# Performance work log

Hardware: AMD Instinct MI355X
Metric: run time of the kernel (lower is better)

The kernel has to match this reference:

```python
import jax, jax.numpy as jnp
import numpy as np

RES = 96
CENTER = RES // 2
EPS = 1e-5


def setup_inputs() -> dict:
    key = jax.random.key(0)
    boundary_2d = jax.random.normal(key, (RES, RES), dtype=jnp.float32)
    return {"boundary_2d": boundary_2d}


def reference(boundary_2d):
    res, center, eps = RES, CENTER, EPS
    idx = jnp.arange(res, dtype=boundary_2d.dtype)
    ii, jj = jnp.meshgrid(idx, idx, indexing="ij")            # [res,res]

    # radius from grid center for every target pixel
    r = jnp.sqrt((ii - center) ** 2 + (jj - center) ** 2)      # [res,res]
    z = center - r + eps                                       # depth into the bulk

    # sources: only strictly-positive boundary values contribute
    w = jnp.where(boundary_2d > 0.0, boundary_2d, 0.0)         # [res,res]

    # all-pairs squared planar distance between targets (i,j) and sources (bi,bj)
    d2 = ((ii[:, :, None, None] - ii[None, None, :, :]) ** 2
          + (jj[:, :, None, None] - jj[None, None, :, :]) ** 2)  # [res,res,res,res]

    # original adds eps to the distance BEFORE squaring: (sqrt(d2)+eps)^2 + z^2
    denom = (jnp.sqrt(d2) + eps) ** 2 + (z ** 2)[:, :, None, None]
    potential = jnp.sum(w[None, None, :, :] / denom, axis=(2, 3))  # [res,res]

    # rim (r >= center-1) passes boundary value through; interior gets the potential
    return jnp.where(r >= center - 1, boundary_2d, potential)
```

## Files before the change

### kernel.cpp

```cpp
#include <hip/hip_runtime.h>

#define RES 96
#define CENTER 48
#define NPIX (RES * RES)
#define EPSF 1e-5f

__global__ __launch_bounds__(256) void topos_kernel(const float* __restrict__ src,
                                                    float* __restrict__ out) {
    const int tid = threadIdx.x;
    const int wave = tid >> 6;
    const int lane = tid & 63;
    const int pix0 = blockIdx.x * 4;
    const int i = pix0 / RES;
    const int j0 = pix0 - i * RES;

    __shared__ float partial[16];

    float z2[4];
    bool allrim = true;
    #pragma unroll
    for (int p = 0; p < 4; ++p) {
        const int dj = j0 + p - CENTER;
        const int r2 = (i - CENTER) * (i - CENTER) + dj * dj;
        allrim &= (r2 >= (CENTER - 1) * (CENTER - 1));
        const float z = (float)CENTER - sqrtf((float)r2) + EPSF;
        z2[p] = z * z;
    }

    if (allrim) {
        if (tid < 4) out[pix0 + tid] = src[pix0 + tid];
        return;
    }

    const int s0 = wave * 256 + lane * 4;
    const int biq0 = s0 / RES;
    const int bjq0 = s0 - biq0 * RES;
    float fdi = (float)(i - biq0);
    float y = (float)(j0 - bjq0);
    const float wraplim = (float)(j0 - 95);
    const float* ptr = src + s0;

    float acc0 = 0.f, acc1 = 0.f, acc2 = 0.f, acc3 = 0.f;

    #pragma unroll 3
    for (int it = 0; it < 9; ++it, ptr += 1024) {
        const float4 b4 = *(const float4*)ptr;
        const float w0 = fmaxf(b4.x, 0.f);
        const float w1 = fmaxf(b4.y, 0.f);
        const float w2 = fmaxf(b4.z, 0.f);
        const float w3 = fmaxf(b4.w, 0.f);

        const float s2 = fdi * fdi;
        const float vm3 = y - 3.f, vm2 = y - 2.f, vm1 = y - 1.f;
        const float vp1 = y + 1.f, vp2 = y + 2.f, vp3 = y + 3.f;

        {
            const float t = s2 + z2[0];
            const float d0 = fmaf(y, y, t),     d1 = fmaf(vm1, vm1, t);
            const float d2 = fmaf(vm2, vm2, t), d3 = fmaf(vm3, vm3, t);
            const float d01 = d0 * d1, d23 = d2 * d3;
            const float n01 = fmaf(w0, d1, w1 * d0);
            const float n23 = fmaf(w2, d3, w3 * d2);
            acc0 = fmaf(fmaf(n01, d23, n23 * d01),
                        __builtin_amdgcn_rcpf(d01 * d23), acc0);
        }
        {
            const float t = s2 + z2[1];
            const float d0 = fmaf(vp1, vp1, t), d1 = fmaf(y, y, t);
            const float d2 = fmaf(vm1, vm1, t), d3 = fmaf(vm2, vm2, t);
            const float d01 = d0 * d1, d23 = d2 * d3;
            const float n01 = fmaf(w0, d1, w1 * d0);
            const float n23 = fmaf(w2, d3, w3 * d2);
            acc1 = fmaf(fmaf(n01, d23, n23 * d01),
                        __builtin_amdgcn_rcpf(d01 * d23), acc1);
        }
        {
            const float t = s2 + z2[2];
            const float d0 = fmaf(vp2, vp2, t), d1 = fmaf(vp1, vp1, t);
            const float d2 = fmaf(y, y, t),     d3 = fmaf(vm1, vm1, t);
            const float d01 = d0 * d1, d23 = d2 * d3;
            const float n01 = fmaf(w0, d1, w1 * d0);
            const float n23 = fmaf(w2, d3, w3 * d2);
            acc2 = fmaf(fmaf(n01, d23, n23 * d01),
                        __builtin_amdgcn_rcpf(d01 * d23), acc2);
        }
        {
            const float t = s2 + z2[3];
            const float d0 = fmaf(vp3, vp3, t), d1 = fmaf(vp2, vp2, t);
            const float d2 = fmaf(vp1, vp1, t), d3 = fmaf(y, y, t);
            const float d01 = d0 * d1, d23 = d2 * d3;
            const float n01 = fmaf(w0, d1, w1 * d0);
            const float n23 = fmaf(w2, d3, w3 * d2);
            acc3 = fmaf(fmaf(n01, d23, n23 * d01),
                        __builtin_amdgcn_rcpf(d01 * d23), acc3);
        }

        y -= 64.f;
        const bool wr = y < wraplim;
        y = wr ? y + 96.f : y;
        fdi -= wr ? 11.f : 10.f;
    }

    #pragma unroll
    for (int off = 32; off > 0; off >>= 1) {
        acc0 += __shfl_down(acc0, off, 64);
        acc1 += __shfl_down(acc1, off, 64);
        acc2 += __shfl_down(acc2, off, 64);
        acc3 += __shfl_down(acc3, off, 64);
    }

    if (lane == 0) {
        partial[wave * 4 + 0] = acc0;
        partial[wave * 4 + 1] = acc1;
        partial[wave * 4 + 2] = acc2;
        partial[wave * 4 + 3] = acc3;
    }
    __syncthreads();

    if (tid < 4) {
        const float sum = (partial[tid] + partial[4 + tid])
                        + (partial[8 + tid] + partial[12 + tid]);
        const int dj = j0 + tid - CENTER;
        const int r2 = (i - CENTER) * (i - CENTER) + dj * dj;
        const bool rim = r2 >= (CENTER - 1) * (CENTER - 1);
        out[pix0 + tid] = rim ? src[pix0 + tid] : sum;
    }
}

extern "C" void kernel_launch(void* const* d_in, const int* in_sizes, int n_in,
                              void* d_out, int out_size, void* d_ws, size_t ws_size,
                              hipStream_t stream) {
    const float* src = (const float*)d_in[0];
    float* out = (float*)d_out;
    topos_kernel<<<NPIX / 4, 256, 0, stream>>>(src, out);
}
```

Baseline: 61.06 us.

## Use 3 waves per block so sources stay row-aligned and prefetch loads

```diff
diff --git a/kernel.cpp b/kernel.cpp
--- a/kernel.cpp
+++ b/kernel.cpp
@@ -5,8 +5,8 @@
 #define NPIX (RES * RES)
 #define EPSF 1e-5f
 
-__global__ __launch_bounds__(256) void topos_kernel(const float* __restrict__ src,
-                                                    float* __restrict__ out) {
+__global__ __launch_bounds__(192, 8) void topos_kernel(const float* __restrict__ src,
+                                                       float* __restrict__ out) {
     const int tid = threadIdx.x;
     const int wave = tid >> 6;
     const int lane = tid & 63;
@@ -14,7 +14,7 @@
     const int i = pix0 / RES;
     const int j0 = pix0 - i * RES;
 
-    __shared__ float partial[16];
+    __shared__ float partial[12];
 
     float z2[4];
     bool allrim = true;
@@ -36,28 +36,35 @@
     const int biq0 = s0 / RES;
     const int bjq0 = s0 - biq0 * RES;
     float fdi = (float)(i - biq0);
-    float y = (float)(j0 - bjq0);
-    const float wraplim = (float)(j0 - 95);
+    const float y = (float)(j0 - bjq0);
+
+    const float um3 = y - 3.f, um2 = y - 2.f, um1 = y - 1.f;
+    const float up1 = y + 1.f, up2 = y + 2.f, up3 = y + 3.f;
+
     const float* ptr = src + s0;
+    float4 b4 = *(const float4*)ptr;
 
     float acc0 = 0.f, acc1 = 0.f, acc2 = 0.f, acc3 = 0.f;
 
     #pragma unroll 3
-    for (int it = 0; it < 9; ++it, ptr += 1024) {
-        const float4 b4 = *(const float4*)ptr;
+    for (int it = 0; it < 12; ++it) {
+        const float* pnext = ptr + (it < 11 ? 768 : 0);
+        const float4 bn = *(const float4*)pnext;
+
         const float w0 = fmaxf(b4.x, 0.f);
         const float w1 = fmaxf(b4.y, 0.f);
         const float w2 = fmaxf(b4.z, 0.f);
         const float w3 = fmaxf(b4.w, 0.f);
 
         const float s2 = fdi * fdi;
-        const float vm3 = y - 3.f, vm2 = y - 2.f, vm1 = y - 1.f;
-        const float vp1 = y + 1.f, vp2 = y + 2.f, vp3 = y + 3.f;
+        const float t0 = s2 + z2[0];
+        const float t1 = s2 + z2[1];
+        const float t2 = s2 + z2[2];
+        const float t3 = s2 + z2[3];
 
         {
-            const float t = s2 + z2[0];
-            const float d0 = fmaf(y, y, t),     d1 = fmaf(vm1, vm1, t);
-            const float d2 = fmaf(vm2, vm2, t), d3 = fmaf(vm3, vm3, t);
+            const float d0 = fmaf(y, y, t0),     d1 = fmaf(um1, um1, t0);
+            const float d2 = fmaf(um2, um2, t0), d3 = fmaf(um3, um3, t0);
             const float d01 = d0 * d1, d23 = d2 * d3;
             const float n01 = fmaf(w0, d1, w1 * d0);
             const float n23 = fmaf(w2, d3, w3 * d2);
@@ -65,9 +72,8 @@
                         __builtin_amdgcn_rcpf(d01 * d23), acc0);
         }
         {
-            const float t = s2 + z2[1];
-            const float d0 = fmaf(vp1, vp1, t), d1 = fmaf(y, y, t);
-            const float d2 = fmaf(vm1, vm1, t), d3 = fmaf(vm2, vm2, t);
+            const float d0 = fmaf(up1, up1, t1), d1 = fmaf(y, y, t1);
+            const float d2 = fmaf(um1, um1, t1), d3 = fmaf(um2, um2, t1);
             const float d01 = d0 * d1, d23 = d2 * d3;
             const float n01 = fmaf(w0, d1, w1 * d0);
             const float n23 = fmaf(w2, d3, w3 * d2);
@@ -75,9 +81,8 @@
                         __builtin_amdgcn_rcpf(d01 * d23), acc1);
         }
         {
-            const float t = s2 + z2[2];
-            const float d0 = fmaf(vp2, vp2, t), d1 = fmaf(vp1, vp1, t);
-            const float d2 = fmaf(y, y, t),     d3 = fmaf(vm1, vm1, t);
+            const float d0 = fmaf(up2, up2, t2), d1 = fmaf(up1, up1, t2);
+            const float d2 = fmaf(y, y, t2),     d3 = fmaf(um1, um1, t2);
             const float d01 = d0 * d1, d23 = d2 * d3;
             const float n01 = fmaf(w0, d1, w1 * d0);
             const float n23 = fmaf(w2, d3, w3 * d2);
@@ -85,9 +90,8 @@
                         __builtin_amdgcn_rcpf(d01 * d23), acc2);
         }
         {
-            const float t = s2 + z2[3];
-            const float d0 = fmaf(vp3, vp3, t), d1 = fmaf(vp2, vp2, t);
-            const float d2 = fmaf(vp1, vp1, t), d3 = fmaf(y, y, t);
+            const float d0 = fmaf(up3, up3, t3), d1 = fmaf(up2, up2, t3);
+            const float d2 = fmaf(up1, up1, t3), d3 = fmaf(y, y, t3);
             const float d01 = d0 * d1, d23 = d2 * d3;
             const float n01 = fmaf(w0, d1, w1 * d0);
             const float n23 = fmaf(w2, d3, w3 * d2);
@@ -95,10 +99,9 @@
                         __builtin_amdgcn_rcpf(d01 * d23), acc3);
         }
 
-        y -= 64.f;
-        const bool wr = y < wraplim;
-        y = wr ? y + 96.f : y;
-        fdi -= wr ? 11.f : 10.f;
+        fdi -= 8.f;
+        ptr = pnext;
+        b4 = bn;
     }
 
     #pragma unroll
@@ -118,8 +121,7 @@
     __syncthreads();
 
     if (tid < 4) {
-        const float sum = (partial[tid] + partial[4 + tid])
-                        + (partial[8 + tid] + partial[12 + tid]);
+        const float sum = partial[tid] + partial[4 + tid] + partial[8 + tid];
         const int dj = j0 + tid - CENTER;
         const int r2 = (i - CENTER) * (i - CENTER) + dj * dj;
         const bool rim = r2 >= (CENTER - 1) * (CENTER - 1);
@@ -132,5 +134,5 @@
                               hipStream_t stream) {
     const float* src = (const float*)d_in[0];
     float* out = (float*)d_out;
-    topos_kernel<<<NPIX / 4, 256, 0, stream>>>(src, out);
+    topos_kernel<<<NPIX / 4, 192, 0, stream>>>(src, out);
 }
```

After: 61.61 us. No clear change (+0.9%).
